# Performance work log

Hardware: AMD Instinct MI355X
Metric: run time of the kernel (lower is better)

## Reference

```python
import jax, jax.numpy as jnp
import numpy as np

B, S, HID, NH, HD, E, K = 8, 1024, 1024, 16, 64, 8, 2
IDIM = 2 * HD  # expert internal dim
EPS = 1e-5


def layer_norm(x, g, b):
    m = jnp.mean(x, axis=-1, keepdims=True)
    v = jnp.mean(jnp.square(x - m), axis=-1, keepdims=True)
    return (x - m) * jax.lax.rsqrt(v + EPS) * g + b


def setup_inputs() -> dict:
    key = jax.random.key(0)
    ks = jax.random.split(key, 12)
    n = jax.random.normal
    return {
        "queries": n(ks[0], (B, S, HID), jnp.float32),
        "keys": n(ks[1], (B, S, HID), jnp.float32),
        "values": n(ks[2], (B, S, HID), jnp.float32),
        "memorys": n(ks[3], (B, NH, S, HD), jnp.float32),
        "Wq": n(ks[4], (HD, HD), jnp.float32) * 0.02,
        "Wk": n(ks[5], (HD, HD), jnp.float32) * 0.02,
        "Wv": n(ks[6], (HD, HD), jnp.float32) * 0.02,
        "forget_gate": n(ks[7], (HD,), jnp.float32),
        "gate_W": n(ks[8], (E, HD), jnp.float32) * 0.02,
        "gate_b": jnp.zeros((E,), jnp.float32),
        "ln1_g": jnp.ones((E, HD), jnp.float32),
        "ln1_b": jnp.zeros((E, HD), jnp.float32),
        "W1": n(ks[9], (E, IDIM, HD), jnp.float32) * 0.02,
        "ln2_g": jnp.ones((E, IDIM), jnp.float32),
        "ln2_b": jnp.zeros((E, IDIM), jnp.float32),
        "W2": n(ks[10], (E, HD, IDIM), jnp.float32) * 0.02,
        "b2": jnp.zeros((E, HD), jnp.float32),
    }


def reference(queries, keys, values, memorys, Wq, Wk, Wv, forget_gate,
              gate_W, gate_b, ln1_g, ln1_b, W1, ln2_g, ln2_b, W2, b2):
    bsz, seq, _ = queries.shape
    gelu = lambda x: jax.nn.gelu(x, approximate=False)

    # head split: [B,S,HID] -> [B,NH,S,HD]
    q = queries.reshape(bsz, seq, NH, HD).transpose(0, 2, 1, 3)
    k = keys.reshape(bsz, seq, NH, HD).transpose(0, 2, 1, 3)
    v = values.reshape(bsz, seq, NH, HD).transpose(0, 2, 1, 3)

    q_ = q @ Wq.T
    k_ = k @ Wk.T
    v_ = v @ Wv.T

    # gated memory cell
    cell = k_ * v_ + forget_gate * memorys
    current_memorys = (1.0 - forget_gate) * cell + forget_gate * memorys
    cell_values = q_ * current_memorys  # [B,NH,S,HD]

    # token-mixing MoE (per-token, over last dim)
    x = cell_values.reshape(-1, HD)  # [N, HD], N = B*NH*S
    logits = x @ gate_W.T + gate_b  # [N, E]
    topv, topi = jax.lax.top_k(logits, K)  # [N, K]
    # sparse combine weights [N, E] (raw gate values, as in the original)
    w = jnp.sum(jax.nn.one_hot(topi, E, dtype=x.dtype) * topv[..., None], axis=1)

    def expert_fwd(g1, b1, w1, g2, b2_, w2, bias2):
        h = gelu(layer_norm(x, g1, b1)) @ w1.T      # [N, IDIM]
        h = gelu(layer_norm(h, g2, b2_)) @ w2.T + bias2  # [N, HD]
        return h

    all_out = jax.vmap(expert_fwd)(ln1_g, ln1_b, W1, ln2_g, ln2_b, W2, b2)  # [E,N,HD]
    moe = jnp.einsum('ne,end->nd', w, all_out)  # [N, HD]

    token_mixing = moe.reshape(bsz, NH, seq, HD).transpose(0, 2, 1, 3).reshape(bsz, seq, NH * HD)
    return token_mixing, current_memorys
```

## Files before the change

### kernel.cpp

```cpp
#include <hip/hip_runtime.h>
#include <stdint.h>

typedef unsigned short u16;
typedef unsigned int   u32;
typedef unsigned long long u64;
typedef __attribute__((ext_vector_type(8))) short short8;
typedef __attribute__((ext_vector_type(4))) short s16x4;
typedef __attribute__((ext_vector_type(4))) float f32x4;

#define B_    8
#define S_    1024
#define HID_  1024
#define NH_   16
#define HD_   64
#define E_    8
#define IDIM_ 128
#define NTOK  (B_*NH_*S_)

#define CSTRIDE 16
#define XROW 65

__device__ __forceinline__ float bf2f(u16 u){ return __uint_as_float(((u32)u) << 16); }
__device__ __forceinline__ u16 f2bf(float f){
    u32 u = __float_as_uint(f);
    u32 r = u + 0x7fffu + ((u >> 16) & 1u);
    return (u16)(r >> 16);
}
__device__ __forceinline__ short8 frag8(const float* __restrict__ p){
    float4 a = *(const float4*)p;
    float4 b = *(const float4*)(p + 4);
    short8 r;
    r[0]=(short)f2bf(a.x); r[1]=(short)f2bf(a.y); r[2]=(short)f2bf(a.z); r[3]=(short)f2bf(a.w);
    r[4]=(short)f2bf(b.x); r[5]=(short)f2bf(b.y); r[6]=(short)f2bf(b.z); r[7]=(short)f2bf(b.w);
    return r;
}
__device__ __forceinline__ float gelu_exact(float x){
    return 0.5f * x * (1.0f + erff(x * 0.70710678118654752f));
}
__device__ __forceinline__ float gelu_f(float x){
    float z = 1.5957691216057308f * (x + 0.044715f * x * x * x);
    float e = __expf(z);
    float t = 1.0f - 2.0f / (e + 1.0f);
    return 0.5f * x * (1.0f + t);
}

__global__ void k_zero(u32* c){
    c[threadIdx.x] = 0;
}

__global__ __launch_bounds__(256) void k_prep(
    const float* __restrict__ W1, const float* __restrict__ W2,
    u16* __restrict__ wB1, u16* __restrict__ wB2, u32* __restrict__ counters)
{
    const int i = blockIdx.x*256 + threadIdx.x;
    if (blockIdx.x == 0) counters[threadIdx.x] = 0;
    wB1[i] = f2bf(W1[i]);
    wB2[i] = f2bf(W2[i]);
}

__global__ __launch_bounds__(256,2) void k_proj(
    const float* __restrict__ qin, const float* __restrict__ kin, const float* __restrict__ vin,
    const float* __restrict__ mem,
    const float* __restrict__ Wq, const float* __restrict__ Wk, const float* __restrict__ Wv,
    const float* __restrict__ fg,
    const float* __restrict__ gW, const float* __restrict__ gB,
    const float* __restrict__ l1g, const float* __restrict__ l1b,
    float* __restrict__ cur_out, float* __restrict__ out0,
    uint4* __restrict__ topiv, u32* __restrict__ counts, int writeXg)
{
    __shared__ float sT[4][64*XROW];
    __shared__ float sGW[512], sGB[8];
    __shared__ float sG1[8*XROW], sB1g[8*XROW];
    __shared__ u32 sWc1[4][8], sWc2[4][8];

    const int tid  = threadIdx.x;
    const int lane = tid & 63;
    const int wid  = tid >> 6;
    const int m    = lane & 15;
    const int kg   = lane >> 4;

    for (int i = tid; i < 512; i += 256){
        sGW[i] = gW[i];
        const int e = i >> 6, d = i & 63;
        sG1[e*XROW+d] = l1g[i]; sB1g[e*XROW+d] = l1b[i];
    }
    if (tid < 8) sGB[tid] = gB[tid];

    const int slab  = blockIdx.x;
    const int chunk = slab & 3, h = (slab >> 2) & 15, b = slab >> 6;
    const int tw    = chunk*256 + wid*64;

    float* sW = &sT[wid][0];

    const float* kbase = kin + ((size_t)b*S_)*HID_ + h*64;
    const float* vbase = vin + ((size_t)b*S_)*HID_ + h*64;
    const float* qbase = qin + ((size_t)b*S_)*HID_ + h*64;

    f32x4 accK[4][4], accV[4][4];
    const f32x4 z = {0.f,0.f,0.f,0.f};
    #pragma unroll
    for (int i=0;i<4;i++){ accK[i][0]=z;accK[i][1]=z;accK[i][2]=z;accK[i][3]=z;
                           accV[i][0]=z;accV[i][1]=z;accV[i][2]=z;accV[i][3]=z; }

    #pragma unroll
    for (int kk=0; kk<2; kk++){
        const int k0 = kk*32 + kg*8;
        short8 aF[4], bF[4];
        #pragma unroll
        for (int mt=0; mt<4; mt++) aF[mt] = frag8(kbase + (size_t)(tw + mt*16 + m)*HID_ + k0);
        #pragma unroll
        for (int ct=0; ct<4; ct++) bF[ct] = frag8(Wk + (ct*16 + m)*64 + k0);
        #pragma unroll
        for (int mt=0; mt<4; mt++)
            #pragma unroll
            for (int ct=0; ct<4; ct++)
                accK[mt][ct] = __builtin_amdgcn_mfma_f32_16x16x32_bf16(aF[mt], bF[ct], accK[mt][ct], 0,0,0);
    }
    #pragma unroll
    for (int kk=0; kk<2; kk++){
        const int k0 = kk*32 + kg*8;
        short8 aF[4], bF[4];
        #pragma unroll
        for (int mt=0; mt<4; mt++) aF[mt] = frag8(vbase + (size_t)(tw + mt*16 + m)*HID_ + k0);
        #pragma unroll
        for (int ct=0; ct<4; ct++) bF[ct] = frag8(Wv + (ct*16 + m)*64 + k0);
        #pragma unroll
        for (int mt=0; mt<4; mt++)
            #pragma unroll
            for (int ct=0; ct<4; ct++)
                accV[mt][ct] = __builtin_amdgcn_mfma_f32_16x16x32_bf16(aF[mt], bF[ct], accV[mt][ct], 0,0,0);
    }

    const size_t nb = ((size_t)(b*NH_ + h)) << 10;
    float fgv[4];
    #pragma unroll
    for (int ct=0; ct<4; ct++) fgv[ct] = fg[ct*16 + m];

    #pragma unroll
    for (int mt=0; mt<4; mt++){
        #pragma unroll
        for (int r=0; r<4; r++){
            const int tok = tw + mt*16 + kg*4 + r;
            const size_t rowo = (nb + (size_t)tok)*64;
            #pragma unroll
            for (int ct=0; ct<4; ct++){
                const int d = ct*16 + m;
                const float kd = accK[mt][ct][r];
                const float vd = accV[mt][ct][r];
                const float f  = fgv[ct];
                const float mv = mem[rowo + d];
                const float cell = kd*vd + f*mv;
                const float cur  = (1.0f - f)*cell + f*mv;
                accK[mt][ct][r] = cur;
                cur_out[rowo + d] = cur;
            }
        }
    }

    f32x4 accQ[4][4];
    #pragma unroll
    for (int i=0;i<4;i++){ accQ[i][0]=z;accQ[i][1]=z;accQ[i][2]=z;accQ[i][3]=z; }

    #pragma unroll
    for (int kk=0; kk<2; kk++){
        const int k0 = kk*32 + kg*8;
        short8 aF[4], bF[4];
        #pragma unroll
        for (int mt=0; mt<4; mt++) aF[mt] = frag8(qbase + (size_t)(tw + mt*16 + m)*HID_ + k0);
        #pragma unroll
        for (int ct=0; ct<4; ct++) bF[ct] = frag8(Wq + (ct*16 + m)*64 + k0);
        #pragma unroll
        for (int mt=0; mt<4; mt++)
            #pragma unroll
            for (int ct=0; ct<4; ct++)
                accQ[mt][ct] = __builtin_amdgcn_mfma_f32_16x16x32_bf16(aF[mt], bF[ct], accQ[mt][ct], 0,0,0);
    }

    if (!writeXg){
        #pragma unroll
        for (int mt=0; mt<4; mt++){
            #pragma unroll
            for (int r=0; r<4; r++){
                const int tok = tw + mt*16 + kg*4 + r;
                const size_t po = ((size_t)(b*S_ + tok)*NH_ + h)*64;
                #pragma unroll
                for (int ct=0; ct<4; ct++){
                    const int d = ct*16 + m;
                    out0[po + d] = accQ[mt][ct][r] * accK[mt][ct][r];
                }
            }
        }
        return;
    }

    __syncthreads();

    #pragma unroll
    for (int mt=0; mt<4; mt++){
        #pragma unroll
        for (int r=0; r<4; r++){
            const int trow = mt*16 + kg*4 + r;
            #pragma unroll
            for (int ct=0; ct<4; ct++){
                const int d = ct*16 + m;
                sW[trow*XROW + d] = accQ[mt][ct][r] * accK[mt][ct][r];
            }
        }
    }

    const int tok = tw + lane;
    const int n   = (int)(nb + tok);
    float rx[64];
    {
        const float* xr = &sW[lane*XROW];
        #pragma unroll
        for (int d = 0; d < 64; d++) rx[d] = xr[d];
    }

    float lg[8];
    #pragma unroll
    for (int e = 0; e < 8; e++) lg[e] = sGB[e];
    float s0 = 0.f, s1 = 0.f;
    #pragma unroll
    for (int d = 0; d < 64; d++){
        const float xv = rx[d];
        s0 += xv; s1 += xv*xv;
        #pragma unroll
        for (int e = 0; e < 8; e++) lg[e] += sGW[e*64 + d] * xv;
    }

    int i1 = 0; float v1 = lg[0];
    #pragma unroll
    for (int e = 1; e < 8; e++){ if (lg[e] > v1){ v1 = lg[e]; i1 = e; } }
    int i2 = -1; float v2 = -3.0e38f;
    #pragma unroll
    for (int e = 0; e < 8; e++){ if (e != i1 && lg[e] > v2){ v2 = lg[e]; i2 = e; } }

    topiv[n] = make_uint4((u32)i1, (u32)i2, __float_as_uint(v1), __float_as_uint(v2));

    #pragma unroll
    for (int e = 0; e < 8; e++){
        u64 m1 = __ballot(i1 == e);
        u64 m2 = __ballot(i2 == e);
        if (lane == 0){ sWc1[wid][e] = (u32)__popcll(m1); sWc2[wid][e] = (u32)__popcll(m2); }
    }

    {
        const float mu = s0 * (1.0f/64.0f);
        const float rs = rsqrtf(s1 * (1.0f/64.0f) - mu*mu + 1e-5f);
        u32* xw = (u32*)&sW[lane*XROW];
        #pragma unroll
        for (int half = 0; half < 2; half++){
            const int ee = half ? i2 : i1;
            const float* g1 = &sG1[ee*XROW];
            const float* b1 = &sB1g[ee*XROW];
            #pragma unroll
            for (int dp = 0; dp < 32; dp++){
                const float v0 = gelu_f((rx[2*dp+0] - mu)*rs*g1[2*dp+0] + b1[2*dp+0]);
                const float vb = gelu_f((rx[2*dp+1] - mu)*rs*g1[2*dp+1] + b1[2*dp+1]);
                xw[half*32 + dp] = (u32)f2bf(v0) | ((u32)f2bf(vb) << 16);
            }
        }
    }

    {
        u16* xgbase = (u16*)out0 + ((nb + (size_t)tw) << 7);
        #pragma unroll
        for (int j = 0; j < 16; j++){
            const int idx = j*64 + lane;
            const int row = idx >> 4, dc = idx & 15;
            const u32* p = (const u32*)&sW[row*XROW] + dc*4;
            uint4 v; v.x = p[0]; v.y = p[1]; v.z = p[2]; v.w = p[3];
            ((uint4*)xgbase)[idx] = v;
        }
    }

    __syncthreads();
    if (tid < 8){
        u32 t = sWc1[0][tid] + sWc1[1][tid] + sWc1[2][tid] + sWc1[3][tid]
              + sWc2[0][tid] + sWc2[1][tid] + sWc2[2][tid] + sWc2[3][tid];
        if (t) atomicAdd(&counts[tid*CSTRIDE], t);
    }
}

__global__ __launch_bounds__(256,2) void k_gate(
    float* __restrict__ x_io, const float* __restrict__ gW, const float* __restrict__ gB,
    const float* __restrict__ l1g, const float* __restrict__ l1b,
    uint4* __restrict__ topiv, u32* __restrict__ counts, int writeXg)
{
    __shared__ float sX[256*XROW];
    __shared__ float sGW[512], sGB[8];
    __shared__ float sG1[8*XROW], sB1g[8*XROW];
    __shared__ u32 sWc[4][8];

    const int tid = threadIdx.x;
    for (int i = tid; i < 512; i += 256){
        sGW[i] = gW[i];
        const int e = i >> 6, d = i & 63;
        sG1[e*XROW+d] = l1g[i]; sB1g[e*XROW+d] = l1b[i];
    }
    if (tid < 8) sGB[tid] = gB[tid];

    const int rowBase = blockIdx.x * 256;
    const float* gsrc = x_io + ((size_t)rowBase << 6);
    #pragma unroll
    for (int j = 0; j < 16; j++){
        const int idx = j*256 + tid;
        const int row = idx >> 4, dc = idx & 15;
        float4 v = ((const float4*)gsrc)[idx];
        float* p = &sX[row*XROW + dc*4];
        p[0]=v.x; p[1]=v.y; p[2]=v.z; p[3]=v.w;
    }
    __syncthreads();

    const int pos = rowBase + tid;
    const int h  = pos & (NH_-1);
    const int bs = pos >> 4;
    const int s  = bs & (S_-1), b = bs >> 10;
    const int n  = ((b*NH_ + h) << 10) + s;

    float rx[64];
    {
        const float* xr = &sX[tid*XROW];
        #pragma unroll
        for (int d = 0; d < 64; d++) rx[d] = xr[d];
    }

    float lg[8];
    #pragma unroll
    for (int e = 0; e < 8; e++) lg[e] = sGB[e];
    float s0 = 0.f, s1 = 0.f;
    #pragma unroll
    for (int d = 0; d < 64; d++){
        const float xv = rx[d];
        s0 += xv; s1 += xv*xv;
        #pragma unroll
        for (int e = 0; e < 8; e++) lg[e] += sGW[e*64 + d] * xv;
    }

    int i1 = 0; float v1 = lg[0];
    #pragma unroll
    for (int e = 1; e < 8; e++){ if (lg[e] > v1){ v1 = lg[e]; i1 = e; } }
    int i2 = -1; float v2 = -3.0e38f;
    #pragma unroll
    for (int e = 0; e < 8; e++){ if (e != i1 && lg[e] > v2){ v2 = lg[e]; i2 = e; } }

    topiv[n] = make_uint4((u32)i1, (u32)i2, __float_as_uint(v1), __float_as_uint(v2));

    {
        const int lane = tid & 63;
        const int w    = tid >> 6;
        #pragma unroll
        for (int e = 0; e < 8; e++){
            u64 m1 = __ballot(i1 == e);
            u64 m2 = __ballot(i2 == e);
            if (lane == 0) sWc[w][e] = (u32)(__popcll(m1) + __popcll(m2));
        }
    }
    __syncthreads();

    if (tid < 8){
        u32 t = sWc[0][tid] + sWc[1][tid] + sWc[2][tid] + sWc[3][tid];
        if (t) atomicAdd(&counts[tid*CSTRIDE], t);
    }
    (void)writeXg;
}

__global__ __launch_bounds__(256,2) void k_scatter(
    const uint4* __restrict__ topiv, const u32* __restrict__ counts, u32* __restrict__ cursors,
    u32* __restrict__ bucket, int2* __restrict__ slots)
{
    __shared__ u32 sC1[4][8], sC2[4][8];
    __shared__ u32 sB1[4][8], sB2w[4][8];

    const int tid = threadIdx.x;
    const int n = blockIdx.x*256 + tid;
    uint4 t = topiv[n];
    const int i1 = (int)t.x, i2 = (int)t.y;

    int off[8]; int acc = 0;
    #pragma unroll
    for (int e = 0; e < 8; e++){ off[e] = acc; acc += (int)counts[e*CSTRIDE]; }

    const int lane = tid & 63;
    const int w    = tid >> 6;
    const u64 low = (1ull << lane) - 1ull;

    u64 myM1 = 0, myM2 = 0;
    #pragma unroll
    for (int e = 0; e < 8; e++){
        u64 m1 = __ballot(i1 == e);
        u64 m2 = __ballot(i2 == e);
        if (i1 == e) myM1 = m1;
        if (i2 == e) myM2 = m2;
        if (lane == 0){ sC1[w][e] = (u32)__popcll(m1); sC2[w][e] = (u32)__popcll(m2); }
    }
    __syncthreads();

    if (tid < 8){
        const int e = tid;
        u32 tot = 0;
        #pragma unroll
        for (int ww = 0; ww < 4; ww++) tot += sC1[ww][e] + sC2[ww][e];
        u32 base = tot ? atomicAdd(&cursors[e*CSTRIDE], tot) : 0;
        u32 run = base;
        #pragma unroll
        for (int ww = 0; ww < 4; ww++){
            sB1[ww][e] = run; run += sC1[ww][e];
            sB2w[ww][e] = run; run += sC2[ww][e];
        }
    }
    __syncthreads();

    const int slot1 = off[i1] + (int)sB1[w][i1] + (int)__popcll(myM1 & low);
    const int slot2 = off[i2] + (int)sB2w[w][i2] + (int)__popcll(myM2 & low);

    bucket[slot1] = ((u32)n << 1);
    bucket[slot2] = ((u32)n << 1) | 1u;
    slots[n] = make_int2(slot1, slot2);
}

__global__ __launch_bounds__(256,4) void k_expert_mfma(
    const float* __restrict__ x_src, const u32* __restrict__ bucket, const u32* __restrict__ counts,
    const u16* __restrict__ wB1, const u16* __restrict__ wB2,
    const float* __restrict__ l2g, const float* __restrict__ l2b,
    const float* __restrict__ b2,  u16* __restrict__ aout)
{
    const int e = blockIdx.x >> 10;
    const int c = blockIdx.x & 1023;
    const int cnt = (int)counts[e*CSTRIDE];
    const int aBase = c * 128;
    if (aBase >= cnt) return;

    int off = 0;
    #pragma unroll
    for (int ee = 0; ee < 8; ee++){ if (ee < e) off += (int)counts[ee*CSTRIDE]; }

    __shared__ __align__(16) u16 sH[4][32*128];
    __shared__ float sL2g[128], sL2b[128], sB2[64];

    const int tid = threadIdx.x;
    if (tid < 128){ sL2g[tid] = l2g[e*128+tid]; sL2b[tid] = l2b[e*128+tid]; }
    else if (tid < 192){ sB2[tid-128] = b2[e*64 + tid-128]; }
    __syncthreads();

    const int lane = tid & 63;
    const int w    = tid >> 6;
    const int m    = lane & 15;
    const int kg   = lane >> 4;
    const int tb   = aBase + w*32;
    char* sHw = (char*)(&sH[w][0]);

    const u16* xg = (const u16*)x_src;
    short8 aF[2][2];
    #pragma unroll
    for (int t = 0; t < 2; t++){
        int a = tb + t*16 + m; if (a > cnt-1) a = cnt-1;
        const u32 bv = bucket[off + a];
        const u16* rp = xg + (((size_t)(bv >> 1)) << 7) + (bv & 1u)*64;
        aF[t][0] = *(const short8*)(rp + kg*8);
        aF[t][1] = *(const short8*)(rp + 32 + kg*8);
    }

    const f32x4 z = {0.f,0.f,0.f,0.f};
    f32x4 acc1[2][8];
    #pragma unroll
    for (int t = 0; t < 2; t++)
        #pragma unroll
        for (int ct = 0; ct < 8; ct++) acc1[t][ct] = z;

    const u16* wB1e = wB1 + e*8192;
    #pragma unroll
    for (int kk = 0; kk < 2; kk++){
        const int k0 = kk*32 + kg*8;
        short8 bF[8];
        #pragma unroll
        for (int ct = 0; ct < 8; ct++)
            bF[ct] = *(const short8*)(wB1e + (ct*16 + m)*64 + k0);
        #pragma unroll
        for (int t = 0; t < 2; t++)
            #pragma unroll
            for (int ct = 0; ct < 8; ct++)
                acc1[t][ct] = __builtin_amdgcn_mfma_f32_16x16x32_bf16(aF[t][kk], bF[ct], acc1[t][ct], 0,0,0);
    }

    #pragma unroll
    for (int t = 0; t < 2; t++){
        #pragma unroll
        for (int r = 0; r < 4; r++){
            float p0 = 0.f, p1 = 0.f;
            #pragma unroll
            for (int ct = 0; ct < 8; ct++){ float v = acc1[t][ct][r]; p0 += v; p1 += v*v; }
            #pragma unroll
            for (int msk = 1; msk < 16; msk <<= 1){
                p0 += __shfl_xor(p0, msk);
                p1 += __shfl_xor(p1, msk);
            }
            const float mu = p0 * (1.0f/128.0f);
            const float rs = rsqrtf(p1 * (1.0f/128.0f) - mu*mu + 1e-5f);
            const int row = t*16 + kg*4 + r;
            #pragma unroll
            for (int ct = 0; ct < 8; ct++){
                const int col = ct*16 + m;
                *(u16*)(sHw + (((row<<8) + (col<<1)) ^ ((row&7)<<4)))
                    = f2bf(gelu_f((acc1[t][ct][r] - mu)*rs*sL2g[col] + sL2b[col]));
            }
        }
    }

    f32x4 acc2[2][4];
    #pragma unroll
    for (int t = 0; t < 2; t++)
        #pragma unroll
        for (int ct = 0; ct < 4; ct++) acc2[t][ct] = z;

    const u16* wB2e = wB2 + e*8192;
    #pragma unroll
    for (int kk = 0; kk < 4; kk++){
        const int k0 = kk*32 + kg*8;
        short8 aF2[2], bF2[4];
        #pragma unroll
        for (int t = 0; t < 2; t++){
            const int row = t*16 + m;
            aF2[t] = *(const short8*)(sHw + (((row<<8) + (k0<<1)) ^ ((row&7)<<4)));
        }
        #pragma unroll
        for (int ct = 0; ct < 4; ct++)
            bF2[ct] = *(const short8*)(wB2e + (ct*16 + m)*128 + k0);
        #pragma unroll
        for (int t = 0; t < 2; t++)
            #pragma unroll
            for (int ct = 0; ct < 4; ct++)
                acc2[t][ct] = __builtin_amdgcn_mfma_f32_16x16x32_bf16(aF2[t], bF2[ct], acc2[t][ct], 0,0,0);
    }

    #pragma unroll
    for (int t = 0; t < 2; t++){
        #pragma unroll
        for (int r = 0; r < 4; r++){
            const int row = t*16 + kg*4 + r;
            #pragma unroll
            for (int ct = 0; ct < 4; ct++){
                const int col = ct*16 + m;
                *(u16*)(sHw + (((row<<7) + (col<<1)) ^ ((row&7)<<4)))
                    = f2bf(acc2[t][ct][r] + sB2[col]);
            }
        }
    }

    #pragma unroll
    for (int it = 0; it < 4; it++){
        const int idx = it*64 + lane;
        const int row = idx >> 3, qq = idx & 7;
        if (tb + row < cnt){
            uint4 v = *(const uint4*)(sHw + (((row<<7) + (qq<<4)) ^ ((row&7)<<4)));
            *(uint4*)(aout + ((size_t)(off + tb + row) << 6) + qq*8) = v;
        }
    }
}

__global__ __launch_bounds__(256,2) void k_expert(
    const float* __restrict__ x_src, const u32* __restrict__ bucket, const u32* __restrict__ counts,
    const float* __restrict__ W1,  const float* __restrict__ W2,
    const float* __restrict__ l1g, const float* __restrict__ l1b,
    const float* __restrict__ l2g, const float* __restrict__ l2b,
    const float* __restrict__ b2,  u16* __restrict__ aout)
{
    const int e = blockIdx.x >> 9;
    const int c = blockIdx.x & 511;
    const int cnt = (int)counts[e*CSTRIDE];
    const int aBase = c * 256;
    if (aBase >= cnt) return;

    int off = 0;
    for (int ee = 0; ee < 8; ee++){ if (ee < e) off += (int)counts[ee*CSTRIDE]; }

    __shared__ float sW1[8192];
    __shared__ float sW2T[128*68];
    __shared__ float sL1g[64], sL1b[64], sL2g[128], sL2b[128], sB2[64];
    const int tid = threadIdx.x;
    for (int i = tid; i < 8192; i += 256){
        sW1[i] = W1[e*8192 + i];
        int d = i >> 7, j = i & 127;
        sW2T[j*68 + d] = W2[e*8192 + i];
    }
    if (tid < 64){ sL1g[tid] = l1g[e*64+tid]; sL1b[tid] = l1b[e*64+tid]; sB2[tid] = b2[e*64+tid]; }
    if (tid < 128){ sL2g[tid] = l2g[e*128+tid]; sL2b[tid] = l2b[e*128+tid]; }
    __syncthreads();

    const int a = aBase + tid;
    if (a >= cnt) return;
    const u32 nv = bucket[off + a] >> 1;
    const int s = (int)(nv & (S_-1));
    const int h = (int)((nv >> 10) & (NH_-1));
    const int b = (int)(nv >> 14);
    const u32 pos32 = (u32)((b*S_ + s)*NH_ + h);

    float g[64];
    #pragma unroll
    for (int i = 0; i < 16; i++){
        float4 t = ((const float4*)(x_src + (size_t)pos32*64))[i];
        g[i*4+0]=t.x; g[i*4+1]=t.y; g[i*4+2]=t.z; g[i*4+3]=t.w;
    }

    float s0 = 0.f, s1 = 0.f;
    #pragma unroll
    for (int d = 0; d < 64; d++){ s0 += g[d]; s1 += g[d]*g[d]; }
    float m  = s0 * (1.0f/64.0f);
    float va = s1 * (1.0f/64.0f) - m*m;
    float rs = rsqrtf(va + 1e-5f);
    #pragma unroll
    for (int d = 0; d < 64; d++) g[d] = gelu_exact((g[d]-m)*rs*sL1g[d] + sL1b[d]);

    u32 hpk[64];
    float hs = 0.f, hs2 = 0.f;
    for (int jp = 0; jp < 64; jp++){
        float h0, h1;
        {
            float a0=0.f,a1=0.f,a2=0.f,a3=0.f;
            const float4* w4 = (const float4*)&sW1[(2*jp)*64];
            #pragma unroll
            for (int i = 0; i < 16; i++){
                float4 ww = w4[i];
                a0 += ww.x*g[i*4+0]; a1 += ww.y*g[i*4+1]; a2 += ww.z*g[i*4+2]; a3 += ww.w*g[i*4+3];
            }
            h0 = (a0+a1)+(a2+a3);
        }
        {
            float a0=0.f,a1=0.f,a2=0.f,a3=0.f;
            const float4* w4 = (const float4*)&sW1[(2*jp+1)*64];
            #pragma unroll
            for (int i = 0; i < 16; i++){
                float4 ww = w4[i];
                a0 += ww.x*g[i*4+0]; a1 += ww.y*g[i*4+1]; a2 += ww.z*g[i*4+2]; a3 += ww.w*g[i*4+3];
            }
            h1 = (a0+a1)+(a2+a3);
        }
        hs += h0 + h1; hs2 += h0*h0 + h1*h1;
        hpk[jp] = (u32)f2bf(h0) | ((u32)f2bf(h1) << 16);
    }
    float m2  = hs  * (1.0f/128.0f);
    float va2 = hs2 * (1.0f/128.0f) - m2*m2;
    float rs2 = rsqrtf(va2 + 1e-5f);

    float acc[64];
    #pragma unroll
    for (int d = 0; d < 64; d++) acc[d] = sB2[d];
    for (int j = 0; j < 128; j++){
        float hj = bf2f((u16)((j & 1) ? (hpk[j>>1] >> 16) : (hpk[j>>1] & 0xffffu)));
        float gh = gelu_exact((hj - m2)*rs2*sL2g[j] + sL2b[j]);
        const float4* w2t = (const float4*)&sW2T[j*68];
        #pragma unroll
        for (int d4 = 0; d4 < 16; d4++){
            float4 w = w2t[d4];
            acc[d4*4+0] += gh * w.x;
            acc[d4*4+1] += gh * w.y;
            acc[d4*4+2] += gh * w.z;
            acc[d4*4+3] += gh * w.w;
        }
    }

    u16* op = aout + (size_t)(off + a) * 64;
    #pragma unroll
    for (int dc = 0; dc < 8; dc++){
        uint4 o;
        o.x = (u32)f2bf(acc[dc*8+0]) | ((u32)f2bf(acc[dc*8+1]) << 16);
        o.y = (u32)f2bf(acc[dc*8+2]) | ((u32)f2bf(acc[dc*8+3]) << 16);
        o.z = (u32)f2bf(acc[dc*8+4]) | ((u32)f2bf(acc[dc*8+5]) << 16);
        o.w = (u32)f2bf(acc[dc*8+6]) | ((u32)f2bf(acc[dc*8+7]) << 16);
        ((uint4*)op)[dc] = o;
    }
}

__global__ __launch_bounds__(256,4) void k_combine(
    const u16* __restrict__ aout, const uint4* __restrict__ topiv,
    const int2* __restrict__ slots, float* __restrict__ out0)
{
    const int tid = threadIdx.x;
    const int p   = blockIdx.x*16 + (tid >> 4);
    const int cq  = tid & 15;

    const int h  = p & (NH_-1);
    const int bs = p >> 4;
    const int b  = bs >> 10, s = bs & (S_-1);
    const int n  = ((b*NH_ + h) << 10) + s;

    uint4 t = topiv[n];
    float w1 = __uint_as_float(t.z), w2 = __uint_as_float(t.w);
    int2 sl = slots[n];

    uint2 ua = *(const uint2*)(aout + (size_t)sl.x*64 + cq*4);
    uint2 ub = *(const uint2*)(aout + (size_t)sl.y*64 + cq*4);

    float4 o;
    o.x = w1*bf2f((u16)(ua.x & 0xffffu)) + w2*bf2f((u16)(ub.x & 0xffffu));
    o.y = w1*bf2f((u16)(ua.x >> 16))     + w2*bf2f((u16)(ub.x >> 16));
    o.z = w1*bf2f((u16)(ua.y & 0xffffu)) + w2*bf2f((u16)(ub.y & 0xffffu));
    o.w = w1*bf2f((u16)(ua.y >> 16))     + w2*bf2f((u16)(ub.y >> 16));
    *(float4*)(out0 + (size_t)p*64 + cq*4) = o;
}

extern "C" void kernel_launch(void* const* d_in, const int* in_sizes, int n_in,
                              void* d_out, int out_size, void* d_ws, size_t ws_size,
                              hipStream_t stream)
{
    const float* qin = (const float*)d_in[0];
    const float* kin = (const float*)d_in[1];
    const float* vin = (const float*)d_in[2];
    const float* mem = (const float*)d_in[3];
    const float* Wq  = (const float*)d_in[4];
    const float* Wk  = (const float*)d_in[5];
    const float* Wv  = (const float*)d_in[6];
    const float* fg  = (const float*)d_in[7];
    const float* gW  = (const float*)d_in[8];
    const float* gB  = (const float*)d_in[9];
    const float* l1g = (const float*)d_in[10];
    const float* l1b = (const float*)d_in[11];
    const float* W1  = (const float*)d_in[12];
    const float* l2g = (const float*)d_in[13];
    const float* l2b = (const float*)d_in[14];
    const float* W2  = (const float*)d_in[15];
    const float* b2  = (const float*)d_in[16];

    float* out0 = (float*)d_out;
    float* out1 = out0 + (size_t)NTOK * 64;

    char* ws = (char*)d_ws;
    u16*   aout   = (u16*)(ws);
    uint4* topiv  = (uint4*)(ws + (size_t)33554432);
    int2*  slots  = (int2*)(ws + (size_t)35651584);
    u32*   bucket = (u32*)(ws + (size_t)36700160);
    u32*   counts = (u32*)(ws + (size_t)37748736);
    u32*   cursors = (u32*)(ws + (size_t)37749248);
    u16*   wB1    = (u16*)(ws + (size_t)37749760);
    u16*   wB2    = (u16*)(ws + (size_t)37880832);
    const size_t WS_NEED = 38011904;

    (void)in_sizes; (void)n_in; (void)out_size;

    const bool use_mfma = (ws_size >= WS_NEED);

    if (use_mfma)
        k_prep <<<256, 256, 0, stream>>>(W1, W2, wB1, wB2, counts);
    else
        k_zero <<<1, 256, 0, stream>>>(counts);
    k_proj   <<<512, 256, 0, stream>>>(qin, kin, vin, mem, Wq, Wk, Wv, fg,
                                       gW, gB, l1g, l1b, out1, out0,
                                       topiv, counts, use_mfma ? 1 : 0);
    if (!use_mfma)
        k_gate <<<NTOK/256, 256, 0, stream>>>(out0, gW, gB, l1g, l1b, topiv, counts, 0);
    k_scatter<<<NTOK/256, 256, 0, stream>>>(topiv, counts, cursors, bucket, slots);
    if (use_mfma)
        k_expert_mfma<<<E_*1024, 256, 0, stream>>>(out0, bucket, counts, wB1, wB2,
                                                   l2g, l2b, b2, aout);
    else
        k_expert <<<E_*512, 256, 0, stream>>>(out0, bucket, counts, W1, W2,
                                              l1g, l1b, l2g, l2b, b2, aout);
    k_combine<<<NTOK/16, 256, 0, stream>>>(aout, topiv, slots, out0);
}
```

Baseline: 302.8 us.

## Fuse weight conversion into scatter and replace atomic expert counts with per-block partials

Removes the separate k_prep launch by having k_scatter convert W1/W2 to bf16. k_proj now writes per-block expert counts to a partial buffer instead of doing global atomicAdds. k_scatter loads all partials and computes totals and per-block prefix offsets itself, which also drops the cursor atomics and the zeroing step. The cost is that every scatter block reads the whole 4096-entry partial table and runs a serial 512-step loop in 8 threads.

```diff
diff --git a/kernel.cpp b/kernel.cpp
--- a/kernel.cpp
+++ b/kernel.cpp
@@ -48,16 +48,6 @@
     c[threadIdx.x] = 0;
 }
 
-__global__ __launch_bounds__(256) void k_prep(
-    const float* __restrict__ W1, const float* __restrict__ W2,
-    u16* __restrict__ wB1, u16* __restrict__ wB2, u32* __restrict__ counters)
-{
-    const int i = blockIdx.x*256 + threadIdx.x;
-    if (blockIdx.x == 0) counters[threadIdx.x] = 0;
-    wB1[i] = f2bf(W1[i]);
-    wB2[i] = f2bf(W2[i]);
-}
-
 __global__ __launch_bounds__(256,2) void k_proj(
     const float* __restrict__ qin, const float* __restrict__ kin, const float* __restrict__ vin,
     const float* __restrict__ mem,
@@ -66,7 +56,7 @@
     const float* __restrict__ gW, const float* __restrict__ gB,
     const float* __restrict__ l1g, const float* __restrict__ l1b,
     float* __restrict__ cur_out, float* __restrict__ out0,
-    uint4* __restrict__ topiv, u32* __restrict__ counts, int writeXg)
+    uint4* __restrict__ topiv, u32* __restrict__ pcount, int writeXg)
 {
     __shared__ float sT[4][64*XROW];
     __shared__ float sGW[512], sGB[8];
@@ -279,7 +269,7 @@
     if (tid < 8){
         u32 t = sWc1[0][tid] + sWc1[1][tid] + sWc1[2][tid] + sWc1[3][tid]
               + sWc2[0][tid] + sWc2[1][tid] + sWc2[2][tid] + sWc2[3][tid];
-        if (t) atomicAdd(&counts[tid*CSTRIDE], t);
+        pcount[blockIdx.x*8 + tid] = t;
     }
 }
 
@@ -367,20 +357,29 @@
 }
 
 __global__ __launch_bounds__(256,2) void k_scatter(
-    const uint4* __restrict__ topiv, const u32* __restrict__ counts, u32* __restrict__ cursors,
-    u32* __restrict__ bucket, int2* __restrict__ slots)
+    const uint4* __restrict__ topiv, u32* __restrict__ counts, u32* __restrict__ cursors,
+    const u32* __restrict__ pc,
+    const float* __restrict__ W1, const float* __restrict__ W2,
+    u16* __restrict__ wB1, u16* __restrict__ wB2,
+    u32* __restrict__ bucket, int2* __restrict__ slots, int useMfma)
 {
     __shared__ u32 sC1[4][8], sC2[4][8];
     __shared__ u32 sB1[4][8], sB2w[4][8];
+    __shared__ u32 pcL[4096];
+    __shared__ u32 sTot[8], sBase[8];
 
     const int tid = threadIdx.x;
-    const int n = blockIdx.x*256 + tid;
+    const int j   = blockIdx.x;
+    const int n   = j*256 + tid;
+
+    if (useMfma){
+        if (n < 65536) wB1[n] = f2bf(W1[n]);
+        else           wB2[n - 65536] = f2bf(W2[n - 65536]);
+        for (int i = tid; i < 4096; i += 256) pcL[i] = pc[i];
+    }
+
     uint4 t = topiv[n];
     const int i1 = (int)t.x, i2 = (int)t.y;
-
-    int off[8]; int acc = 0;
-    #pragma unroll
-    for (int e = 0; e < 8; e++){ off[e] = acc; acc += (int)counts[e*CSTRIDE]; }
 
     const int lane = tid & 63;
     const int w    = tid >> 6;
@@ -397,23 +396,54 @@
     }
     __syncthreads();
 
-    if (tid < 8){
-        const int e = tid;
-        u32 tot = 0;
-        #pragma unroll
-        for (int ww = 0; ww < 4; ww++) tot += sC1[ww][e] + sC2[ww][e];
-        u32 base = tot ? atomicAdd(&cursors[e*CSTRIDE], tot) : 0;
-        u32 run = base;
-        #pragma unroll
-        for (int ww = 0; ww < 4; ww++){
-            sB1[ww][e] = run; run += sC1[ww][e];
-            sB2w[ww][e] = run; run += sC2[ww][e];
-        }
-    }
-    __syncthreads();
-
-    const int slot1 = off[i1] + (int)sB1[w][i1] + (int)__popcll(myM1 & low);
-    const int slot2 = off[i2] + (int)sB2w[w][i2] + (int)__popcll(myM2 & low);
+    if (useMfma){
+        if (tid < 8){
+            const int e = tid;
+            u32 tot = 0, base = 0;
+            for (int i = 0; i < 512; i++){
+                const u32 c = pcL[i*8 + e];
+                tot += c;
+                if (i < j) base += c;
+            }
+            sTot[e] = tot; sBase[e] = base;
+            if (j == 0) counts[e*CSTRIDE] = tot;
+        }
+        __syncthreads();
+        if (tid < 8){
+            const int e = tid;
+            u32 off = 0;
+            #pragma unroll
+            for (int ee = 0; ee < 8; ee++){ if (ee < e) off += sTot[ee]; }
+            u32 run = off + sBase[e];
+            #pragma unroll
+            for (int ww = 0; ww < 4; ww++){
+                sB1[ww][e] = run; run += sC1[ww][e];
+                sB2w[ww][e] = run; run += sC2[ww][e];
+            }
+        }
+        __syncthreads();
+    } else {
+        int off[8]; int acc = 0;
+        #pragma unroll
+        for (int e = 0; e < 8; e++){ off[e] = acc; acc += (int)counts[e*CSTRIDE]; }
+        if (tid < 8){
+            const int e = tid;
+            u32 tot = 0;
+            #pragma unroll
+            for (int ww = 0; ww < 4; ww++) tot += sC1[ww][e] + sC2[ww][e];
+            u32 base = tot ? atomicAdd(&cursors[e*CSTRIDE], tot) : 0;
+            u32 run = (u32)off[e] + base;
+            #pragma unroll
+            for (int ww = 0; ww < 4; ww++){
+                sB1[ww][e] = run; run += sC1[ww][e];
+                sB2w[ww][e] = run; run += sC2[ww][e];
+            }
+        }
+        __syncthreads();
+    }
+
+    const int slot1 = (int)sB1[w][i1] + (int)__popcll(myM1 & low);
+    const int slot2 = (int)sB2w[w][i2] + (int)__popcll(myM2 & low);
 
     bucket[slot1] = ((u32)n << 1);
     bucket[slot2] = ((u32)n << 1) | 1u;
@@ -727,6 +757,7 @@
 
     char* ws = (char*)d_ws;
     u16*   aout   = (u16*)(ws);
+    u32*   pc     = (u32*)(ws);
     uint4* topiv  = (uint4*)(ws + (size_t)33554432);
     int2*  slots  = (int2*)(ws + (size_t)35651584);
     u32*   bucket = (u32*)(ws + (size_t)36700160);
@@ -740,21 +771,25 @@
 
     const bool use_mfma = (ws_size >= WS_NEED);
 
-    if (use_mfma)
-        k_prep <<<256, 256, 0, stream>>>(W1, W2, wB1, wB2, counts);
-    else
-        k_zero <<<1, 256, 0, stream>>>(counts);
-    k_proj   <<<512, 256, 0, stream>>>(qin, kin, vin, mem, Wq, Wk, Wv, fg,
-                                       gW, gB, l1g, l1b, out1, out0,
-                                       topiv, counts, use_mfma ? 1 : 0);
-    if (!use_mfma)
-        k_gate <<<NTOK/256, 256, 0, stream>>>(out0, gW, gB, l1g, l1b, topiv, counts, 0);
-    k_scatter<<<NTOK/256, 256, 0, stream>>>(topiv, counts, cursors, bucket, slots);
-    if (use_mfma)
+    if (use_mfma){
+        k_proj   <<<512, 256, 0, stream>>>(qin, kin, vin, mem, Wq, Wk, Wv, fg,
+                                           gW, gB, l1g, l1b, out1, out0,
+                                           topiv, pc, 1);
+        k_scatter<<<512, 256, 0, stream>>>(topiv, counts, cursors, pc,
+                                           W1, W2, wB1, wB2, bucket, slots, 1);
         k_expert_mfma<<<E_*1024, 256, 0, stream>>>(out0, bucket, counts, wB1, wB2,
                                                    l2g, l2b, b2, aout);
-    else
+        k_combine<<<NTOK/16, 256, 0, stream>>>(aout, topiv, slots, out0);
+    } else {
+        k_zero   <<<1, 256, 0, stream>>>(counts);
+        k_proj   <<<512, 256, 0, stream>>>(qin, kin, vin, mem, Wq, Wk, Wv, fg,
+                                           gW, gB, l1g, l1b, out1, out0,
+                                           topiv, pc, 0);
+        k_gate   <<<NTOK/256, 256, 0, stream>>>(out0, gW, gB, l1g, l1b, topiv, counts, 0);
+        k_scatter<<<NTOK/256, 256, 0, stream>>>(topiv, counts, cursors, pc,
+                                                W1, W2, wB1, wB2, bucket, slots, 0);
         k_expert <<<E_*512, 256, 0, stream>>>(out0, bucket, counts, W1, W2,
                                               l1g, l1b, l2g, l2b, b2, aout);
-    k_combine<<<NTOK/16, 256, 0, stream>>>(aout, topiv, slots, out0);
-}
+        k_combine<<<NTOK/16, 256, 0, stream>>>(aout, topiv, slots, out0);
+    }
+}
```

New measurement: 300.4 us, median of 4. Within noise of the previous version (-0.8%).
